# Optimization experiments

Hardware: AMD Instinct MI355X
Metric: run time of the kernel (lower is better)

## Reference

```python
import jax, jax.numpy as jnp
import numpy as np

SIM_T = 32  # simulation_length


def uniform_spikes(rates, T):
    """Faithful port of to_uniform_spikes, vectorized over all T cycles.
    rates: (B, D) in [0,1] -> spike train (T, B, D) of {0,1} floats."""
    N = jnp.round(rates * T).astype(jnp.int32)          # (B, D)
    cycles = jnp.arange(T, dtype=jnp.float32)[:, None, None]  # (T,1,1)
    N_safe = jnp.maximum(N, 1)
    spacing = T / N_safe.astype(jnp.float32)
    mask = (N != 0) & (N != T)                          # cycle < T always holds here
    res = mask & (jnp.floor(cycles / spacing) < N_safe) & (jnp.floor(jnp.mod(cycles, spacing)) == 0)
    res = res.astype(jnp.float32)
    res = jnp.where(N == T, jnp.float32(1.0), res)      # result[N == T] = 1.0
    return res


def lif_core(spikes_in, weight, threshold):
    """LIF integration: memb += inp @ W.T; fired = threshold < memb; Default reset.
    spikes_in: (T, B, in); weight: (out, in). Returns (T, B, out) spike train."""
    B = spikes_in.shape[1]
    out_dim = weight.shape[0]

    def step(memb, s):
        memb = memb + s @ weight.T
        fired = threshold < memb                        # thresholding_mode '<'
        memb = jnp.where(fired, memb - threshold, memb) # firing_mode 'Default'
        return memb, fired.astype(jnp.float32)

    _, out_train = jax.lax.scan(step, jnp.zeros((B, out_dim), spikes_in.dtype), spikes_in)
    return out_train


def setup_inputs() -> dict:
    key = jax.random.key(0)
    k = jax.random.split(key, 8)
    B, D_in = 64, 4096
    x = jax.random.uniform(k[0], (B, D_in), dtype=jnp.float32)          # rates in [0,1]
    w0 = jax.random.normal(k[1], (4096, 4096), dtype=jnp.float32) / np.sqrt(4096.0)
    t0 = jnp.float32(1.0)
    w2 = jax.random.normal(k[2], (1000, 1024), dtype=jnp.float32) / np.sqrt(1024.0)
    t2 = jnp.float32(1.0)
    idx0 = jax.random.permutation(k[3], 4096).astype(jnp.int32)
    idx1 = jax.random.permutation(k[4], 4096).astype(jnp.int32)
    idx2 = jax.random.permutation(k[5], 1024).astype(jnp.int32)
    idx_out = jnp.arange(1000, dtype=jnp.int32)
    return {"x": x, "w0": w0, "t0": t0, "w2": w2, "t2": t2,
            "idx0": idx0, "idx1": idx1, "idx2": idx2, "idx_out": idx_out}


def reference(x, w0, t0, w2, t2, idx0, idx1, idx2, idx_out):
    B = x.shape[0]
    T = SIM_T
    # Input encoding (Uniform spike mode), train shape (T, B, 4096)
    inp_train = uniform_spikes(x, T)
    # NeuralCore 0: per-source gather + LIF
    s0 = lif_core(inp_train[:, :, idx0], w0, t0)        # (T, B, 4096)
    # ComputeOp avg_pool2d: sync barrier -> rates over full window
    rates = s0[:, :, idx1].mean(axis=0)                 # (B, 4096)
    C, H, W = 64, 8, 8
    xr = rates.reshape(B, C, H, W)
    pooled = xr.reshape(B, C, H // 2, 2, W // 2, 2).mean(axis=(3, 5))  # (B, 64, 4, 4)
    y_rates = jnp.clip(pooled.reshape(B, -1), 0.0, 1.0) # (B, 1024)
    s1 = uniform_spikes(y_rates, T)                     # (T, B, 1024)
    # NeuralCore 2
    s2 = lif_core(s1[:, :, idx2], w2, t2)               # (T, B, 1000)
    # Output accumulation over cycles (spike counts)
    return s2[:, :, idx_out].sum(axis=0)                # (B, 1000)
```

## Files before the change

### kernel.cpp

```cpp
#include <hip/hip_runtime.h>
#include <stdint.h>
#include <stddef.h>

#define D0 4096
#define D1 1024
#define NOUT 1000
#define NB 64

constexpr uint32_t spike_pattern_ct(int N) {
  if (N <= 0) return 0u;
  if (N >= 32) return 0xFFFFFFFFu;
  float sp = 32.0f / (float)N;
  uint32_t m = 0;
  for (int c = 0; c < 32; ++c) {
    double q = (double)c / (double)sp;
    int n = (int)q;
    double r = (double)c - (double)n * (double)sp;
    if (r < 1.0) m |= (1u << c);
  }
  return m;
}

__global__ void transpose_w0_k(const float* __restrict__ w, float* __restrict__ wt) {
  __shared__ float tile[32][33];
  int j0 = blockIdx.x * 32;
  int o0 = blockIdx.y * 32;
  int tx = threadIdx.x, ty = threadIdx.y;
  float4 v = *reinterpret_cast<const float4*>(&w[(size_t)(o0 + ty) * D0 + j0 + 4 * tx]);
  tile[ty][4 * tx + 0] = v.x;
  tile[ty][4 * tx + 1] = v.y;
  tile[ty][4 * tx + 2] = v.z;
  tile[ty][4 * tx + 3] = v.w;
  __syncthreads();
  float4 u;
  u.x = tile[4 * tx + 0][ty];
  u.y = tile[4 * tx + 1][ty];
  u.z = tile[4 * tx + 2][ty];
  u.w = tile[4 * tx + 3][ty];
  *reinterpret_cast<float4*>(&wt[(size_t)(j0 + ty) * D0 + o0 + 4 * tx]) = u;
}

__global__ void transpose_w2_k(const float* __restrict__ w, float* __restrict__ wt) {
  __shared__ float tile[32][33];
  int j0 = blockIdx.x * 32;
  int o0 = blockIdx.y * 32;
  int tx = threadIdx.x, ty = threadIdx.y;
  int o = o0 + ty;
  float4 v = make_float4(0.f, 0.f, 0.f, 0.f);
  if (o < NOUT) v = *reinterpret_cast<const float4*>(&w[(size_t)o * D1 + j0 + 4 * tx]);
  tile[ty][4 * tx + 0] = v.x;
  tile[ty][4 * tx + 1] = v.y;
  tile[ty][4 * tx + 2] = v.z;
  tile[ty][4 * tx + 3] = v.w;
  __syncthreads();
  float4 u;
  u.x = tile[4 * tx + 0][ty];
  u.y = tile[4 * tx + 1][ty];
  u.z = tile[4 * tx + 2][ty];
  u.w = tile[4 * tx + 3][ty];
  *reinterpret_cast<float4*>(&wt[(size_t)(j0 + ty) * D1 + o0 + 4 * tx]) = u;
}

__global__ void compute_N0_k(const float* __restrict__ x, int* __restrict__ N0) {
  int i = blockIdx.x * 256 + threadIdx.x;
  N0[i] = (int)rintf(x[i] * 32.0f);
}

template <int D>
__global__ void prep_sort_k(const int* __restrict__ Nsrc, const int* __restrict__ idx,
                            uint32_t* __restrict__ perm, int* __restrict__ starts) {
  __shared__ int keys[D];
  __shared__ int hist[33];
  __shared__ int base[34];
  __shared__ int cursor[33];
  int b = blockIdx.x;
  int tid = threadIdx.x;
  if (tid < 33) hist[tid] = 0;
  __syncthreads();
  for (int j = tid; j < D; j += 256) {
    int k = Nsrc[b * D + idx[j]];
    keys[j] = k;
    atomicAdd(&hist[k], 1);
  }
  __syncthreads();
  if (tid == 0) {
    int s = 0;
    for (int k = 0; k < 33; ++k) { base[k] = s; cursor[k] = s; s += hist[k]; }
    base[33] = s;
  }
  __syncthreads();
  if (tid < 34) starts[b * 34 + tid] = base[tid];
  for (int j = tid; j < D; j += 256) {
    int k = keys[j];
    int pos = atomicAdd(&cursor[k], 1);
    perm[b * D + pos] = (uint32_t)j;
  }
}

template <int D, int OSTRIDE, int TILES>
__launch_bounds__(512, 4)
__global__ void lif_core_k(const float* __restrict__ wt, const uint32_t* __restrict__ perm,
                           const int* __restrict__ starts, const float* __restrict__ thr_p,
                           int* __restrict__ cnt_out) {
  __shared__ double cshare[16][256];
  int tid = threadIdx.x;
  int b = blockIdx.y;
  int col = tid & 255;
  int half = __builtin_amdgcn_readfirstlane(tid >> 8);

  const uint32_t* permb = perm + (size_t)b * D;
  const int* st = starts + b * 34;
  double th = (double)thr_p[0];

  for (int zt = 0; zt < TILES; ++zt) {
    int o = (blockIdx.x + gridDim.x * zt) * 256 + col;

    double bs[33];
#pragma unroll
    for (int k = 1; k <= 32; ++k) bs[k] = 0.0;

#pragma unroll
    for (int k = 1; k <= 32; ++k) {
      int s = __builtin_amdgcn_readfirstlane(st[k]);
      int e = __builtin_amdgcn_readfirstlane(st[k + 1]);
      if (s == e) continue;
      int mid = s + ((e - s) >> 1);
      int i  = half ? mid : s;
      int i1 = half ? e : mid;
      double a0 = 0.0, a1 = 0.0, a2 = 0.0, a3 = 0.0;
      for (; i + 8 <= i1; i += 8) {
        int j0 = __builtin_amdgcn_readfirstlane((int)permb[i + 0]);
        int j1 = __builtin_amdgcn_readfirstlane((int)permb[i + 1]);
        int j2 = __builtin_amdgcn_readfirstlane((int)permb[i + 2]);
        int j3 = __builtin_amdgcn_readfirstlane((int)permb[i + 3]);
        int j4 = __builtin_amdgcn_readfirstlane((int)permb[i + 4]);
        int j5 = __builtin_amdgcn_readfirstlane((int)permb[i + 5]);
        int j6 = __builtin_amdgcn_readfirstlane((int)permb[i + 6]);
        int j7 = __builtin_amdgcn_readfirstlane((int)permb[i + 7]);
        float f0 = wt[(size_t)(uint32_t)j0 * OSTRIDE + o];
        float f1 = wt[(size_t)(uint32_t)j1 * OSTRIDE + o];
        float f2 = wt[(size_t)(uint32_t)j2 * OSTRIDE + o];
        float f3 = wt[(size_t)(uint32_t)j3 * OSTRIDE + o];
        float f4 = wt[(size_t)(uint32_t)j4 * OSTRIDE + o];
        float f5 = wt[(size_t)(uint32_t)j5 * OSTRIDE + o];
        float f6 = wt[(size_t)(uint32_t)j6 * OSTRIDE + o];
        float f7 = wt[(size_t)(uint32_t)j7 * OSTRIDE + o];
        a0 += (double)f0; a1 += (double)f1; a2 += (double)f2; a3 += (double)f3;
        a0 += (double)f4; a1 += (double)f5; a2 += (double)f6; a3 += (double)f7;
      }
      for (; i < i1; ++i) {
        int j = __builtin_amdgcn_readfirstlane((int)permb[i]);
        a0 += (double)wt[(size_t)(uint32_t)j * OSTRIDE + o];
      }
      bs[k] = (a0 + a1) + (a2 + a3);
    }

    __syncthreads();
    if (half) {
#pragma unroll
      for (int k = 1; k <= 16; ++k) cshare[k - 1][col] = bs[k];
    }
    __syncthreads();
    if (!half) {
#pragma unroll
      for (int k = 1; k <= 16; ++k) bs[k] += cshare[k - 1][col];
    }
    __syncthreads();
    if (half) {
#pragma unroll
      for (int k = 17; k <= 32; ++k) cshare[k - 17][col] = bs[k];
    }
    __syncthreads();
    if (!half) {
#pragma unroll
      for (int k = 17; k <= 32; ++k) bs[k] += cshare[k - 17][col];

      double memb = 0.0;
      int cnt = 0;
#pragma unroll
      for (int t = 0; t < 32; ++t) {
#pragma unroll
        for (int k = 1; k <= 32; ++k)
          if ((spike_pattern_ct(k) >> t) & 1u) memb += bs[k];
        if (memb > th) { memb -= th; ++cnt; }
      }
      cnt_out[(size_t)b * OSTRIDE + o] = cnt;
    }
  }
}

__global__ void pool_encode_k(const int* __restrict__ k0, const int* __restrict__ idx1,
                              int* __restrict__ N1) {
  int i = blockIdx.x * 256 + threadIdx.x;
  int b = i >> 10;
  int q2 = i & 1023;
  int c = q2 >> 4;
  int h2 = (q2 >> 2) & 3;
  int w2 = q2 & 3;
  int cnt = 0;
#pragma unroll
  for (int dh = 0; dh < 2; ++dh)
#pragma unroll
    for (int dw = 0; dw < 2; ++dw) {
      int q = c * 64 + (2 * h2 + dh) * 8 + (2 * w2 + dw);
      cnt += k0[b * D0 + idx1[q]];
    }
  N1[i] = (int)rintf((float)cnt * 0.25f);
}

__global__ void write_out_k(const int* __restrict__ cnt2, const int* __restrict__ idx_out,
                            float* __restrict__ out) {
  int i = blockIdx.x * 256 + threadIdx.x;
  if (i >= NB * NOUT) return;
  int b = i / NOUT;
  int r = i - b * NOUT;
  out[i] = (float)cnt2[b * D1 + idx_out[r]];
}

extern "C" void kernel_launch(void* const* d_in, const int* in_sizes, int n_in,
                              void* d_out, int out_size, void* d_ws, size_t ws_size,
                              hipStream_t stream) {
  const float* x      = (const float*)d_in[0];
  const float* w0     = (const float*)d_in[1];
  const float* t0     = (const float*)d_in[2];
  const float* w2     = (const float*)d_in[3];
  const float* t2     = (const float*)d_in[4];
  const int*   idx0   = (const int*)d_in[5];
  const int*   idx1   = (const int*)d_in[6];
  const int*   idx2   = (const int*)d_in[7];
  const int*   idx_out= (const int*)d_in[8];
  float* out = (float*)d_out;

  char* ws = (char*)d_ws;
  float*    w0T    = (float*)ws;    ws += (size_t)D0 * D0 * 4;
  float*    w2T    = (float*)ws;    ws += (size_t)D1 * D1 * 4;
  uint32_t* perm0  = (uint32_t*)ws; ws += (size_t)NB * D0 * 4;
  uint32_t* perm2  = (uint32_t*)ws; ws += (size_t)NB * D1 * 4;
  int*      N0     = (int*)ws;      ws += (size_t)NB * D0 * 4;
  int*      N1     = (int*)ws;      ws += (size_t)NB * D1 * 4;
  int*      k0     = (int*)ws;      ws += (size_t)NB * D0 * 4;
  int*      cnt2   = (int*)ws;      ws += (size_t)NB * D1 * 4;
  int*      starts0= (int*)ws;      ws += (size_t)NB * 34 * 4;
  int*      starts2= (int*)ws;      ws += (size_t)NB * 34 * 4;

  transpose_w0_k<<<dim3(D0 / 32, D0 / 32), dim3(8, 32), 0, stream>>>(w0, w0T);
  transpose_w2_k<<<dim3(D1 / 32, D1 / 32), dim3(8, 32), 0, stream>>>(w2, w2T);
  compute_N0_k<<<NB * D0 / 256, 256, 0, stream>>>(x, N0);
  prep_sort_k<D0><<<NB, 256, 0, stream>>>(N0, idx0, perm0, starts0);
  lif_core_k<D0, D0, 2><<<dim3(8, NB, 1), 512, 0, stream>>>(w0T, perm0, starts0, t0, k0);
  pool_encode_k<<<NB * D1 / 256, 256, 0, stream>>>(k0, idx1, N1);
  prep_sort_k<D1><<<NB, 256, 0, stream>>>(N1, idx2, perm2, starts2);
  lif_core_k<D1, D1, 1><<<dim3(4, NB, 1), 512, 0, stream>>>(w2T, perm2, starts2, t2, cnt2);
  write_out_k<<<(NB * NOUT + 255) / 256, 256, 0, stream>>>(cnt2, idx_out, out);
}
```

Baseline: 439.9 us.

## Fuse encode into sort kernels, stage 16-bit permutation in LDS

The rate-encoding kernels (compute_N0 and pool_encode) are folded into the per-batch counting-sort kernels, which removes two launches and the intermediate N buffers. The permutation is stored as 16-bit indices and copied once into shared memory at the start of each LIF block, so the inner loop reads indices from LDS rather than global memory. The extra LDS (8 KB for D0) may lower occupancy, and the fused sort kernels now do the encoding work with only 64 blocks.

```diff
diff --git a/kernel.cpp b/kernel.cpp
--- a/kernel.cpp
+++ b/kernel.cpp
@@ -61,15 +61,9 @@
   *reinterpret_cast<float4*>(&wt[(size_t)(j0 + ty) * D1 + o0 + 4 * tx]) = u;
 }
 
-__global__ void compute_N0_k(const float* __restrict__ x, int* __restrict__ N0) {
-  int i = blockIdx.x * 256 + threadIdx.x;
-  N0[i] = (int)rintf(x[i] * 32.0f);
-}
-
-template <int D>
-__global__ void prep_sort_k(const int* __restrict__ Nsrc, const int* __restrict__ idx,
-                            uint32_t* __restrict__ perm, int* __restrict__ starts) {
-  __shared__ int keys[D];
+__global__ void prep_sort0_k(const float* __restrict__ x, const int* __restrict__ idx0,
+                             uint16_t* __restrict__ perm, int* __restrict__ starts) {
+  __shared__ int keys[D0];
   __shared__ int hist[33];
   __shared__ int base[34];
   __shared__ int cursor[33];
@@ -77,8 +71,8 @@
   int tid = threadIdx.x;
   if (tid < 33) hist[tid] = 0;
   __syncthreads();
-  for (int j = tid; j < D; j += 256) {
-    int k = Nsrc[b * D + idx[j]];
+  for (int j = tid; j < D0; j += 256) {
+    int k = (int)rintf(x[b * D0 + idx0[j]] * 32.0f);
     keys[j] = k;
     atomicAdd(&hist[k], 1);
   }
@@ -90,25 +84,75 @@
   }
   __syncthreads();
   if (tid < 34) starts[b * 34 + tid] = base[tid];
-  for (int j = tid; j < D; j += 256) {
+  for (int j = tid; j < D0; j += 256) {
     int k = keys[j];
     int pos = atomicAdd(&cursor[k], 1);
-    perm[b * D + pos] = (uint32_t)j;
+    perm[b * D0 + pos] = (uint16_t)j;
+  }
+}
+
+__global__ void prep_sort1_k(const int* __restrict__ k0, const int* __restrict__ idx1,
+                             const int* __restrict__ idx2,
+                             uint16_t* __restrict__ perm, int* __restrict__ starts) {
+  __shared__ int keys[D1];
+  __shared__ int hist[33];
+  __shared__ int base[34];
+  __shared__ int cursor[33];
+  int b = blockIdx.x;
+  int tid = threadIdx.x;
+  if (tid < 33) hist[tid] = 0;
+  __syncthreads();
+  for (int j = tid; j < D1; j += 256) {
+    int q2 = idx2[j];
+    int c = q2 >> 4;
+    int h2 = (q2 >> 2) & 3;
+    int w2 = q2 & 3;
+    int cnt = 0;
+#pragma unroll
+    for (int dh = 0; dh < 2; ++dh)
+#pragma unroll
+      for (int dw = 0; dw < 2; ++dw) {
+        int q = c * 64 + (2 * h2 + dh) * 8 + (2 * w2 + dw);
+        cnt += k0[b * D0 + idx1[q]];
+      }
+    int k = (int)rintf((float)cnt * 0.25f);
+    keys[j] = k;
+    atomicAdd(&hist[k], 1);
+  }
+  __syncthreads();
+  if (tid == 0) {
+    int s = 0;
+    for (int k = 0; k < 33; ++k) { base[k] = s; cursor[k] = s; s += hist[k]; }
+    base[33] = s;
+  }
+  __syncthreads();
+  if (tid < 34) starts[b * 34 + tid] = base[tid];
+  for (int j = tid; j < D1; j += 256) {
+    int k = keys[j];
+    int pos = atomicAdd(&cursor[k], 1);
+    perm[b * D1 + pos] = (uint16_t)j;
   }
 }
 
 template <int D, int OSTRIDE, int TILES>
 __launch_bounds__(512, 4)
-__global__ void lif_core_k(const float* __restrict__ wt, const uint32_t* __restrict__ perm,
+__global__ void lif_core_k(const float* __restrict__ wt, const uint16_t* __restrict__ perm,
                            const int* __restrict__ starts, const float* __restrict__ thr_p,
                            int* __restrict__ cnt_out) {
   __shared__ double cshare[16][256];
+  __shared__ uint16_t permS[D];
   int tid = threadIdx.x;
   int b = blockIdx.y;
   int col = tid & 255;
   int half = __builtin_amdgcn_readfirstlane(tid >> 8);
 
-  const uint32_t* permb = perm + (size_t)b * D;
+  {
+    const ushort2* p2 = reinterpret_cast<const ushort2*>(perm + (size_t)b * D);
+    ushort2* s2 = reinterpret_cast<ushort2*>(permS);
+    for (int i = tid; i < D / 2; i += 512) s2[i] = p2[i];
+  }
+  __syncthreads();
+
   const int* st = starts + b * 34;
   double th = (double)thr_p[0];
 
@@ -129,14 +173,14 @@
       int i1 = half ? e : mid;
       double a0 = 0.0, a1 = 0.0, a2 = 0.0, a3 = 0.0;
       for (; i + 8 <= i1; i += 8) {
-        int j0 = __builtin_amdgcn_readfirstlane((int)permb[i + 0]);
-        int j1 = __builtin_amdgcn_readfirstlane((int)permb[i + 1]);
-        int j2 = __builtin_amdgcn_readfirstlane((int)permb[i + 2]);
-        int j3 = __builtin_amdgcn_readfirstlane((int)permb[i + 3]);
-        int j4 = __builtin_amdgcn_readfirstlane((int)permb[i + 4]);
-        int j5 = __builtin_amdgcn_readfirstlane((int)permb[i + 5]);
-        int j6 = __builtin_amdgcn_readfirstlane((int)permb[i + 6]);
-        int j7 = __builtin_amdgcn_readfirstlane((int)permb[i + 7]);
+        int j0 = __builtin_amdgcn_readfirstlane((int)permS[i + 0]);
+        int j1 = __builtin_amdgcn_readfirstlane((int)permS[i + 1]);
+        int j2 = __builtin_amdgcn_readfirstlane((int)permS[i + 2]);
+        int j3 = __builtin_amdgcn_readfirstlane((int)permS[i + 3]);
+        int j4 = __builtin_amdgcn_readfirstlane((int)permS[i + 4]);
+        int j5 = __builtin_amdgcn_readfirstlane((int)permS[i + 5]);
+        int j6 = __builtin_amdgcn_readfirstlane((int)permS[i + 6]);
+        int j7 = __builtin_amdgcn_readfirstlane((int)permS[i + 7]);
         float f0 = wt[(size_t)(uint32_t)j0 * OSTRIDE + o];
         float f1 = wt[(size_t)(uint32_t)j1 * OSTRIDE + o];
         float f2 = wt[(size_t)(uint32_t)j2 * OSTRIDE + o];
@@ -149,7 +193,7 @@
         a0 += (double)f4; a1 += (double)f5; a2 += (double)f6; a3 += (double)f7;
       }
       for (; i < i1; ++i) {
-        int j = __builtin_amdgcn_readfirstlane((int)permb[i]);
+        int j = __builtin_amdgcn_readfirstlane((int)permS[i]);
         a0 += (double)wt[(size_t)(uint32_t)j * OSTRIDE + o];
       }
       bs[k] = (a0 + a1) + (a2 + a3);
@@ -187,25 +231,6 @@
       cnt_out[(size_t)b * OSTRIDE + o] = cnt;
     }
   }
-}
-
-__global__ void pool_encode_k(const int* __restrict__ k0, const int* __restrict__ idx1,
-                              int* __restrict__ N1) {
-  int i = blockIdx.x * 256 + threadIdx.x;
-  int b = i >> 10;
-  int q2 = i & 1023;
-  int c = q2 >> 4;
-  int h2 = (q2 >> 2) & 3;
-  int w2 = q2 & 3;
-  int cnt = 0;
-#pragma unroll
-  for (int dh = 0; dh < 2; ++dh)
-#pragma unroll
-    for (int dw = 0; dw < 2; ++dw) {
-      int q = c * 64 + (2 * h2 + dh) * 8 + (2 * w2 + dw);
-      cnt += k0[b * D0 + idx1[q]];
-    }
-  N1[i] = (int)rintf((float)cnt * 0.25f);
 }
 
 __global__ void write_out_k(const int* __restrict__ cnt2, const int* __restrict__ idx_out,
@@ -234,10 +259,8 @@
   char* ws = (char*)d_ws;
   float*    w0T    = (float*)ws;    ws += (size_t)D0 * D0 * 4;
   float*    w2T    = (float*)ws;    ws += (size_t)D1 * D1 * 4;
-  uint32_t* perm0  = (uint32_t*)ws; ws += (size_t)NB * D0 * 4;
-  uint32_t* perm2  = (uint32_t*)ws; ws += (size_t)NB * D1 * 4;
-  int*      N0     = (int*)ws;      ws += (size_t)NB * D0 * 4;
-  int*      N1     = (int*)ws;      ws += (size_t)NB * D1 * 4;
+  uint16_t* perm0  = (uint16_t*)ws; ws += (size_t)NB * D0 * 2;
+  uint16_t* perm2  = (uint16_t*)ws; ws += (size_t)NB * D1 * 2;
   int*      k0     = (int*)ws;      ws += (size_t)NB * D0 * 4;
   int*      cnt2   = (int*)ws;      ws += (size_t)NB * D1 * 4;
   int*      starts0= (int*)ws;      ws += (size_t)NB * 34 * 4;
@@ -245,11 +268,9 @@
 
   transpose_w0_k<<<dim3(D0 / 32, D0 / 32), dim3(8, 32), 0, stream>>>(w0, w0T);
   transpose_w2_k<<<dim3(D1 / 32, D1 / 32), dim3(8, 32), 0, stream>>>(w2, w2T);
-  compute_N0_k<<<NB * D0 / 256, 256, 0, stream>>>(x, N0);
-  prep_sort_k<D0><<<NB, 256, 0, stream>>>(N0, idx0, perm0, starts0);
+  prep_sort0_k<<<NB, 256, 0, stream>>>(x, idx0, perm0, starts0);
   lif_core_k<D0, D0, 2><<<dim3(8, NB, 1), 512, 0, stream>>>(w0T, perm0, starts0, t0, k0);
-  pool_encode_k<<<NB * D1 / 256, 256, 0, stream>>>(k0, idx1, N1);
-  prep_sort_k<D1><<<NB, 256, 0, stream>>>(N1, idx2, perm2, starts2);
+  prep_sort1_k<<<NB, 256, 0, stream>>>(k0, idx1, idx2, perm2, starts2);
   lif_core_k<D1, D1, 1><<<dim3(4, NB, 1), 512, 0, stream>>>(w2T, perm2, starts2, t2, cnt2);
   write_out_k<<<(NB * NOUT + 255) / 256, 256, 0, stream>>>(cnt2, idx_out, out);
 }
```

Result: no change. 432.6 us (-1.6%).
